# Kernel optimization log

Measured on AMD Instinct MI355X. Metric: run time of the kernel, lower is better.

Reference implementation:

```python
import jax, jax.numpy as jnp
import numpy as np
from jax import lax

T_STEPS = 4
TAU = 2.0
V_THRESHOLD = 1.0
V_RESET = 0.0
ATAN_ALPHA = 2.0

@jax.custom_vjp
def atan_spike(x):
    # Heaviside forward, ATan surrogate gradient (spikingjelly surrogate.ATan, alpha=2)
    return (x >= 0.0).astype(x.dtype)

def _atan_fwd(x):
    return atan_spike(x), x

def _atan_bwd(x, g):
    grad = (ATAN_ALPHA / 2.0) / (1.0 + (jnp.pi / 2.0 * ATAN_ALPHA * x) ** 2)
    return (g * grad,)

atan_spike.defvjp(_atan_fwd, _atan_bwd)

def setup_inputs() -> dict:
    key = jax.random.key(0)
    inputs = jax.random.normal(key, (32, 720, 862), dtype=jnp.float32)  # B, L, C
    return {"inputs": inputs}

def reference(inputs) -> jnp.ndarray:
    # repeat along a new leading time dim: (T, B, L, C)
    x = jnp.broadcast_to(inputs[None], (T_STEPS,) + inputs.shape)
    # permute(0,1,3,2) -> (T, B, C, L)
    x = jnp.transpose(x, (0, 1, 3, 2))

    def step(v, xt):
        # LIF with decay_input=True (spikingjelly default):
        # v <- v + (x - (v - v_reset)) / tau
        v = v + (xt - (v - V_RESET)) / TAU
        s = atan_spike(v - V_THRESHOLD)
        sd = lax.stop_gradient(s)  # detach_reset=True
        v = (1.0 - sd) * v + sd * V_RESET  # hard reset
        return v, s

    v0 = jnp.zeros_like(x[0])
    _, spks = lax.scan(step, v0, x)
    return spks  # (T, B, C, L)
```

## Files before the change

### kernel.cpp

```cpp
#include <hip/hip_runtime.h>


#define B_DIM 32
#define L_DIM 720
#define C_DIM 862
#define T_STEPS 4
#define TC 16
#define SLB 724

typedef float v2f __attribute__((ext_vector_type(2)));
typedef float v4f __attribute__((ext_vector_type(4)));

__device__ __forceinline__ unsigned lif_spike_byte(float x) {
    float v = 0.0f;
    unsigned b = 0;
#pragma unroll
    for (int t = 0; t < T_STEPS; ++t) {
        v += (x - v) * 0.5f;
        if (v >= 1.0f) { b |= (1u << t); v = 0.0f; }
    }
    return b;
}

__global__ __launch_bounds__(256)
void lif_repeat_encoder(const float* __restrict__ in, float* __restrict__ out) {
    __shared__ unsigned char sl[TC * SLB];

    const int b   = blockIdx.y;
    const int c0  = blockIdx.x * TC;
    const int tid = threadIdx.x;

    const float* __restrict__ inb = in + (size_t)b * (L_DIM * C_DIM);

    {
        const int cl2 = (tid & 7) << 1;
        const int c   = c0 + cl2;
        const int r0  = tid >> 3;
        if (c < C_DIM) {
            for (int base = 0; base < L_DIM; base += 128) {
                v2f v[4];
#pragma unroll
                for (int u = 0; u < 4; ++u) {
                    const int r = base + r0 + 32 * u;
                    if (r < L_DIM)
                        v[u] = *(const v2f*)(inb + (size_t)r * C_DIM + c);
                }
#pragma unroll
                for (int u = 0; u < 4; ++u) {
                    const int r = base + r0 + 32 * u;
                    if (r < L_DIM) {
                        sl[cl2 * SLB + r]       = (unsigned char)lif_spike_byte(v[u].x);
                        sl[(cl2 + 1) * SLB + r] = (unsigned char)lif_spike_byte(v[u].y);
                    }
                }
            }
        }
    }
    __syncthreads();

    const int wave = tid >> 6;
    const int lane = tid & 63;

    unsigned sp[4][3];
#pragma unroll
    for (int q = 0; q < 4; ++q) {
#pragma unroll
        for (int round = 0; round < 3; ++round) {
            const int j = lane + 64 * round;
            const int cl = 4 * wave + q;
            sp[q][round] = (j < L_DIM / 4)
                ? *(const unsigned*)(sl + cl * SLB + 4 * j) : 0u;
        }
    }

    const size_t plane = (size_t)B_DIM * C_DIM * L_DIM;

#pragma unroll
    for (int t = 0; t < T_STEPS; ++t) {
#pragma unroll
        for (int q = 0; q < 4; ++q) {
            const int c = c0 + 4 * wave + q;
            if (c >= C_DIM) continue;
            float* dst = out + (size_t)t * plane + ((size_t)b * C_DIM + c) * L_DIM;
#pragma unroll
            for (int round = 0; round < 3; ++round) {
                const int j = lane + 64 * round;
                if (j >= L_DIM / 4) break;
                const unsigned y = (sp[q][round] >> t) & 0x01010101u;
                v4f o;
                o.x = (float)(y & 1u);
                o.y = (float)((y >> 8) & 1u);
                o.z = (float)((y >> 16) & 1u);
                o.w = (float)((y >> 24) & 1u);
                *(v4f*)(dst + 4 * j) = o;
            }
        }
    }
}

extern "C" void kernel_launch(void* const* d_in, const int* in_sizes, int n_in,
                              void* d_out, int out_size, void* d_ws, size_t ws_size,
                              hipStream_t stream) {
    const float* in = (const float*)d_in[0];
    float* out = (float*)d_out;

    dim3 block(256, 1, 1);
    dim3 grid((C_DIM + TC - 1) / TC,
              B_DIM,
              1);

    lif_repeat_encoder<<<grid, block, 0, stream>>>(in, out);
}
```

Measured before the change: 374.9 us.

## Widen channel tile, pack spike bytes into word LDS writes, flatten output stores

The channel tile doubles to 32. In the load phase each thread now reads four consecutive rows and packs their spike bytes into 32-bit words, so it does one word write to LDS per channel instead of separate byte writes. In the store phase each wave takes 8 contiguous channels and treats their output as one flat contiguous run of 1440 float4 values. This keeps all lanes busy and removes the partial rounds that occurred per channel. The aim is fewer LDS transactions and more regular, fully coalesced writes, at the cost of more registers per thread and half as many blocks.

```diff
diff --git a/kernel.cpp b/kernel.cpp
--- a/kernel.cpp
+++ b/kernel.cpp
@@ -5,7 +5,7 @@
 #define L_DIM 720
 #define C_DIM 862
 #define T_STEPS 4
-#define TC 16
+#define TC 32
 #define SLB 724
 
 typedef float v2f __attribute__((ext_vector_type(2)));
@@ -33,26 +33,27 @@
     const float* __restrict__ inb = in + (size_t)b * (L_DIM * C_DIM);
 
     {
-        const int cl2 = (tid & 7) << 1;
-        const int c   = c0 + cl2;
-        const int r0  = tid >> 3;
-        if (c < C_DIM) {
-            for (int base = 0; base < L_DIM; base += 128) {
-                v2f v[4];
+        const int c2 = tid & 15;
+        const int rg = tid >> 4;
+        const int cl = 2 * c2;
+        const int c  = c0 + cl;
+        const bool cok = (c + 1) < C_DIM;
+
+        for (int P = 0; P < 12; ++P) {
+            const int rbase = 64 * P + 4 * rg;
+            if (cok && rbase < L_DIM) {
+                v2f x[4];
+#pragma unroll
+                for (int u = 0; u < 4; ++u)
+                    x[u] = *(const v2f*)(inb + (size_t)(rbase + u) * C_DIM + c);
+                unsigned p0 = 0, p1 = 0;
 #pragma unroll
                 for (int u = 0; u < 4; ++u) {
-                    const int r = base + r0 + 32 * u;
-                    if (r < L_DIM)
-                        v[u] = *(const v2f*)(inb + (size_t)r * C_DIM + c);
+                    p0 |= lif_spike_byte(x[u].x) << (8 * u);
+                    p1 |= lif_spike_byte(x[u].y) << (8 * u);
                 }
-#pragma unroll
-                for (int u = 0; u < 4; ++u) {
-                    const int r = base + r0 + 32 * u;
-                    if (r < L_DIM) {
-                        sl[cl2 * SLB + r]       = (unsigned char)lif_spike_byte(v[u].x);
-                        sl[(cl2 + 1) * SLB + r] = (unsigned char)lif_spike_byte(v[u].y);
-                    }
-                }
+                *(unsigned*)(sl + cl * SLB + rbase)       = p0;
+                *(unsigned*)(sl + (cl + 1) * SLB + rbase) = p1;
             }
         }
     }
@@ -60,39 +61,51 @@
 
     const int wave = tid >> 6;
     const int lane = tid & 63;
+    const int row0 = 8 * wave;
 
-    unsigned sp[4][3];
+    unsigned sp[23];
 #pragma unroll
-    for (int q = 0; q < 4; ++q) {
-#pragma unroll
-        for (int round = 0; round < 3; ++round) {
-            const int j = lane + 64 * round;
-            const int cl = 4 * wave + q;
-            sp[q][round] = (j < L_DIM / 4)
-                ? *(const unsigned*)(sl + cl * SLB + 4 * j) : 0u;
-        }
+    for (int k = 0; k < 23; ++k) {
+        const int s = lane + 64 * k;
+        sp[k] = (s < 1440)
+            ? *(const unsigned*)(sl + (row0 + s / 180) * SLB + 4 * (s % 180))
+            : 0u;
     }
 
     const size_t plane = (size_t)B_DIM * C_DIM * L_DIM;
+    const bool full = (c0 + TC) <= C_DIM;
+    float* const dst0 = out + ((size_t)b * C_DIM + c0 + row0) * L_DIM;
 
 #pragma unroll
     for (int t = 0; t < T_STEPS; ++t) {
+        float* const dstt = dst0 + (size_t)t * plane;
+        if (full) {
 #pragma unroll
-        for (int q = 0; q < 4; ++q) {
-            const int c = c0 + 4 * wave + q;
-            if (c >= C_DIM) continue;
-            float* dst = out + (size_t)t * plane + ((size_t)b * C_DIM + c) * L_DIM;
-#pragma unroll
-            for (int round = 0; round < 3; ++round) {
-                const int j = lane + 64 * round;
-                if (j >= L_DIM / 4) break;
-                const unsigned y = (sp[q][round] >> t) & 0x01010101u;
+            for (int k = 0; k < 23; ++k) {
+                const int s = lane + 64 * k;
+                if (s >= 1440) break;
+                const unsigned y = (sp[k] >> t) & 0x01010101u;
                 v4f o;
                 o.x = (float)(y & 1u);
                 o.y = (float)((y >> 8) & 1u);
                 o.z = (float)((y >> 16) & 1u);
                 o.w = (float)((y >> 24) & 1u);
-                *(v4f*)(dst + 4 * j) = o;
+                *(v4f*)(dstt + 4 * (size_t)s) = o;
+            }
+        } else {
+#pragma unroll
+            for (int k = 0; k < 23; ++k) {
+                const int s = lane + 64 * k;
+                if (s >= 1440) break;
+                const int cl = s / 180;
+                if (c0 + row0 + cl >= C_DIM) continue;
+                const unsigned y = (sp[k] >> t) & 0x01010101u;
+                v4f o;
+                o.x = (float)(y & 1u);
+                o.y = (float)((y >> 8) & 1u);
+                o.z = (float)((y >> 16) & 1u);
+                o.w = (float)((y >> 24) & 1u);
+                *(v4f*)(dstt + 4 * (size_t)s) = o;
             }
         }
     }
```

Result: no change. 370.6 us (-1.1%).
